# Performance work log

Hardware: AMD Instinct MI355X
Metric: run time of the kernel (lower is better)

## Reference

```python
import jax, jax.numpy as jnp
import numpy as np

SPLINE_ORDER = 3


def _bspline_basis(x, knots, k, order):
    """Cox-de Boor recursion with static (python float) knots, matching the torch code exactly."""
    if order == 0:
        if k + 1 >= len(knots):
            return jnp.zeros_like(x)
        return ((knots[k] <= x) & (x < knots[k + 1])).astype(x.dtype)
    left = 0.0
    right = 0.0
    if k + order < len(knots) and knots[k + order] != knots[k]:
        left = (x - knots[k]) / (knots[k + order] - knots[k]) * _bspline_basis(x, knots, k, order - 1)
    if k + order + 1 < len(knots) and knots[k + order + 1] != knots[k + 1]:
        right = (knots[k + order + 1] - x) / (knots[k + order + 1] - knots[k + 1]) * _bspline_basis(x, knots, k + 1, order - 1)
    return left + right


def setup_inputs() -> dict:
    key = jax.random.key(0)
    k1, k2, k3 = jax.random.split(key, 3)
    B, S, IN, OUT, NUM_KNOTS = 16, 4096, 256, 256, 5
    x = jax.random.normal(k1, (B, S, IN), dtype=jnp.float32)
    inner_coeffs = jax.random.normal(k2, (IN, NUM_KNOTS), dtype=jnp.float32) * 0.1
    outer_coeffs = jax.random.normal(k3, (OUT, IN), dtype=jnp.float32) * 0.1
    return {"x": x, "inner_coeffs": inner_coeffs, "outer_coeffs": outer_coeffs}


def reference(x, inner_coeffs, outer_coeffs):
    in_dim, num_knots = inner_coeffs.shape
    # knots = linspace(-1, 1, num_knots + spline_order), static python floats
    knots = np.linspace(-1.0, 1.0, num_knots + SPLINE_ORDER).tolist()
    xt = jnp.tanh(x)  # [B, S, I]
    # Original loops k in range(num_knots - spline_order); remaining basis columns stay zero,
    # so only the first n_active inner coefficients contribute.
    n_active = num_knots - SPLINE_ORDER
    basis = jnp.stack(
        [_bspline_basis(xt, knots, k, SPLINE_ORDER) for k in range(n_active)], axis=-1
    )  # [B, S, I, n_active]
    inner = jnp.einsum('bsik,ik->bsi', basis, inner_coeffs[:, :n_active])  # [B, S, I]
    return jnp.einsum('bsi,oi->bso', inner, outer_coeffs)  # [B, S, O]
```

## Files before the change

kernel.cpp:

```cpp
#include <hip/hip_runtime.h>
#include <hip/hip_bf16.h>
#include <stdint.h>


typedef __attribute__((ext_vector_type(8))) short short8;
typedef __attribute__((ext_vector_type(4))) float f32x4;

__device__ __forceinline__ uint16_t f2bf(float f) {
    union { float f; uint32_t u; } v; v.f = f;
    uint32_t r = v.u + 0x7FFFu + ((v.u >> 16) & 1u);
    return (uint16_t)(r >> 16);
}

__device__ __forceinline__ float cube_relu(float v) {
    float m = fmaxf(v, 0.0f);
    return m * m * m;
}

__device__ __forceinline__ float inner_eval(float xx, float c0, float c1) {
    float e  = __expf(2.0f * xx);
    float t  = 1.0f - 2.0f * __builtin_amdgcn_rcpf(e + 1.0f);
    float u  = (t + 1.0f) * 3.5f;
    float w0 = cube_relu(u);
    float w1 = cube_relu(u - 1.0f);
    float w2 = cube_relu(u - 2.0f);
    float w3 = cube_relu(u - 3.0f);
    float w4 = cube_relu(u - 4.0f);
    float w5 = cube_relu(u - 5.0f);
    float B0 = w0 - 4.0f*w1 + 6.0f*w2 - 4.0f*w3 + w4;
    float B1 = w1 - 4.0f*w2 + 6.0f*w3 - 4.0f*w4 + w5;
    return (c0 * B0 + c1 * B1) * (1.0f / 6.0f);
}

__device__ __forceinline__ void load_lds16(const void* g, void* l) {
    __builtin_amdgcn_global_load_lds(
        (const __attribute__((address_space(1))) uint32_t*)g,
        (__attribute__((address_space(3))) uint32_t*)l, 16, 0, 0);
}

__global__ void conv_w(const float4* __restrict__ wf, uint2* __restrict__ o) {
    const int i = blockIdx.x * blockDim.x + threadIdx.x;
    const float4 v = wf[i];
    uint2 r;
    r.x = (uint32_t)f2bf(v.x) | ((uint32_t)f2bf(v.y) << 16);
    r.y = (uint32_t)f2bf(v.z) | ((uint32_t)f2bf(v.w) << 16);
    o[i] = r;
}

#define SMEM_BYTES 22528

__global__ void kan_fused(const float* __restrict__ x,
                          const float* __restrict__ ic,
                          const uint16_t* __restrict__ wb,
                          float* __restrict__ out)
{
    __shared__ __align__(16) char smem[SMEM_BYTES];
    uint16_t* A_lds  = (uint16_t*)smem;
    char*     B_base = smem + 4096;
    float2*   C2     = (float2*)(smem + 20480);

    const int t    = threadIdx.x;
    const int lane = t & 63;
    const int w    = t >> 6;
    const int m0   = blockIdx.x * 64;

    C2[t] = make_float2(ic[t * 5 + 0], ic[t * 5 + 1]);

    f32x4 acc[4][4];
    #pragma unroll
    for (int i = 0; i < 4; ++i)
        #pragma unroll
        for (int j = 0; j < 4; ++j)
            acc[i][j] = (f32x4){0.f, 0.f, 0.f, 0.f};

    const int rowA = t >> 3;
    const int colA = (t & 7) << 2;
    const int mrow = lane & 15;
    const int quad = lane >> 4;

    #pragma unroll 1
    for (int kk = 0; kk < 8; ++kk) {
        __syncthreads();

        #pragma unroll
        for (int j = 0; j < 4; ++j) {
            const int f = ((w * 4 + j) << 10) + lane * 16;
            const int r = f >> 6;
            const int q = (f >> 4) & 3;
            load_lds16(wb + r * 256 + kk * 32 + q * 8, B_base + f);
        }

        #pragma unroll
        for (int j = 0; j < 2; ++j) {
            const int r  = rowA + j * 32;
            const int gk = kk * 32 + colA;
            const float4 xv = *(const float4*)(x + (size_t)(m0 + r) * 256 + gk);
            const float4 cA = *(const float4*)(&C2[gk]);
            const float4 cB = *(const float4*)(&C2[gk + 2]);
            float v0 = inner_eval(xv.x, cA.x, cA.y);
            float v1 = inner_eval(xv.y, cA.z, cA.w);
            float v2 = inner_eval(xv.z, cB.x, cB.y);
            float v3 = inner_eval(xv.w, cB.z, cB.w);
            uint32_t p0 = (uint32_t)f2bf(v0) | ((uint32_t)f2bf(v1) << 16);
            uint32_t p1 = (uint32_t)f2bf(v2) | ((uint32_t)f2bf(v3) << 16);
            *(uint2*)((char*)A_lds + (r * 32 + colA) * 2) = make_uint2(p0, p1);
        }

        __syncthreads();

        short8 a[4], b[4];
        #pragma unroll
        for (int i = 0; i < 4; ++i) {
            a[i] = *(const short8*)((const char*)A_lds + ((i * 16 + mrow) * 32 + quad * 8) * 2);
            b[i] = *(const short8*)(B_base + ((w * 64 + i * 16 + mrow) * 32 + quad * 8) * 2);
        }
        #pragma unroll
        for (int i = 0; i < 4; ++i)
            #pragma unroll
            for (int j = 0; j < 4; ++j)
                acc[i][j] = __builtin_amdgcn_mfma_f32_16x16x32_bf16(a[i], b[j], acc[i][j], 0, 0, 0);
    }

    #pragma unroll
    for (int i = 0; i < 4; ++i) {
        #pragma unroll
        for (int r = 0; r < 4; ++r) {
            const size_t row = (size_t)(m0 + i * 16 + quad * 4 + r);
            float* orow = out + row * 256 + w * 64 + mrow;
            #pragma unroll
            for (int j = 0; j < 4; ++j)
                orow[j * 16] = acc[i][j][r];
        }
    }
}

extern "C" void kernel_launch(void* const* d_in, const int* in_sizes, int n_in,
                              void* d_out, int out_size, void* d_ws, size_t ws_size,
                              hipStream_t stream) {
    const float* x  = (const float*)d_in[0];
    const float* ic = (const float*)d_in[1];
    const float* oc = (const float*)d_in[2];
    uint16_t* wb = (uint16_t*)d_ws;

    conv_w<<<64, 256, 0, stream>>>((const float4*)oc, (uint2*)wb);
    kan_fused<<<1024, 256, 0, stream>>>(x, ic, wb, (float*)d_out);
}
```

Measured before the change: 141.9 us.

## Drop LDS staging; each wave computes 16 rows by 256 outputs from registers

Reorganizes the fused kernel so each wave owns 16 rows and all 256 output columns. A-fragments come from the spline evaluation directly in registers, and B-fragments are loaded straight from global/L2 into registers. This removes the LDS A/B tiles and the per-iteration __syncthreads. The x loads are software-prefetched one k-step ahead, and packing uses the hardware bf16x2 conversion. In exchange each wave re-reads the entire weight matrix from L2, and the spline work is no longer shared across waves, which raises register pressure and cache traffic.

```diff
diff --git a/kernel.cpp b/kernel.cpp
--- a/kernel.cpp
+++ b/kernel.cpp
@@ -10,6 +10,12 @@
     union { float f; uint32_t u; } v; v.f = f;
     uint32_t r = v.u + 0x7FFFu + ((v.u >> 16) & 1u);
     return (uint16_t)(r >> 16);
+}
+
+__device__ __forceinline__ uint32_t pack_bf2(float lo, float hi) {
+    __hip_bfloat162 h = __float22bfloat162_rn(make_float2(lo, hi));
+    union { __hip_bfloat162 h; uint32_t u; } v; v.h = h;
+    return v.u;
 }
 
 __device__ __forceinline__ float cube_relu(float v) {
@@ -32,12 +38,6 @@
     return (c0 * B0 + c1 * B1) * (1.0f / 6.0f);
 }
 
-__device__ __forceinline__ void load_lds16(const void* g, void* l) {
-    __builtin_amdgcn_global_load_lds(
-        (const __attribute__((address_space(1))) uint32_t*)g,
-        (__attribute__((address_space(3))) uint32_t*)l, 16, 0, 0);
-}
-
 __global__ void conv_w(const float4* __restrict__ wf, uint2* __restrict__ o) {
     const int i = blockIdx.x * blockDim.x + threadIdx.x;
     const float4 v = wf[i];
@@ -47,90 +47,80 @@
     o[i] = r;
 }
 
-#define SMEM_BYTES 22528
-
-__global__ void kan_fused(const float* __restrict__ x,
-                          const float* __restrict__ ic,
-                          const uint16_t* __restrict__ wb,
-                          float* __restrict__ out)
+__global__ void __launch_bounds__(256) kan_fused(const float* __restrict__ x,
+                                                 const float* __restrict__ ic,
+                                                 const uint16_t* __restrict__ wb,
+                                                 float* __restrict__ out)
 {
-    __shared__ __align__(16) char smem[SMEM_BYTES];
-    uint16_t* A_lds  = (uint16_t*)smem;
-    char*     B_base = smem + 4096;
-    float2*   C2     = (float2*)(smem + 20480);
+    __shared__ __align__(16) float2 C2[256];
 
     const int t    = threadIdx.x;
     const int lane = t & 63;
     const int w    = t >> 6;
-    const int m0   = blockIdx.x * 64;
+    const int mrow = lane & 15;
+    const int quad = lane >> 4;
+    const int m    = blockIdx.x * 64 + w * 16 + mrow;
 
     C2[t] = make_float2(ic[t * 5 + 0], ic[t * 5 + 1]);
+    __syncthreads();
 
-    f32x4 acc[4][4];
+    f32x4 acc[16];
     #pragma unroll
-    for (int i = 0; i < 4; ++i)
-        #pragma unroll
-        for (int j = 0; j < 4; ++j)
-            acc[i][j] = (f32x4){0.f, 0.f, 0.f, 0.f};
+    for (int j = 0; j < 16; ++j) acc[j] = (f32x4){0.f, 0.f, 0.f, 0.f};
 
-    const int rowA = t >> 3;
-    const int colA = (t & 7) << 2;
-    const int mrow = lane & 15;
-    const int quad = lane >> 4;
+    const float*    xp = x  + (size_t)m * 256 + quad * 8;
+    const uint16_t* wp = wb + mrow * 256 + quad * 8;
+
+    float4 xa = *(const float4*)(xp + 0);
+    float4 xb = *(const float4*)(xp + 4);
 
     #pragma unroll 1
     for (int kk = 0; kk < 8; ++kk) {
-        __syncthreads();
+        short8 b[16];
+        #pragma unroll
+        for (int j = 0; j < 16; ++j)
+            b[j] = *(const short8*)(wp + j * 4096 + kk * 32);
+
+        float4 xa_n = xa, xb_n = xb;
+        if (kk < 7) {
+            xa_n = *(const float4*)(xp + kk * 32 + 32);
+            xb_n = *(const float4*)(xp + kk * 32 + 36);
+        }
+
+        const int gk = kk * 32 + quad * 8;
+        const float4 cA = *(const float4*)(&C2[gk + 0]);
+        const float4 cB = *(const float4*)(&C2[gk + 2]);
+        const float4 cC = *(const float4*)(&C2[gk + 4]);
+        const float4 cD = *(const float4*)(&C2[gk + 6]);
+
+        float v0 = inner_eval(xa.x, cA.x, cA.y);
+        float v1 = inner_eval(xa.y, cA.z, cA.w);
+        float v2 = inner_eval(xa.z, cB.x, cB.y);
+        float v3 = inner_eval(xa.w, cB.z, cB.w);
+        float v4 = inner_eval(xb.x, cC.x, cC.y);
+        float v5 = inner_eval(xb.y, cC.z, cC.w);
+        float v6 = inner_eval(xb.z, cD.x, cD.y);
+        float v7 = inner_eval(xb.w, cD.z, cD.w);
+
+        union { short8 v; uint32_t u[4]; } af;
+        af.u[0] = pack_bf2(v0, v1);
+        af.u[1] = pack_bf2(v2, v3);
+        af.u[2] = pack_bf2(v4, v5);
+        af.u[3] = pack_bf2(v6, v7);
 
         #pragma unroll
-        for (int j = 0; j < 4; ++j) {
-            const int f = ((w * 4 + j) << 10) + lane * 16;
-            const int r = f >> 6;
-            const int q = (f >> 4) & 3;
-            load_lds16(wb + r * 256 + kk * 32 + q * 8, B_base + f);
-        }
+        for (int j = 0; j < 16; ++j)
+            acc[j] = __builtin_amdgcn_mfma_f32_16x16x32_bf16(af.v, b[j], acc[j], 0, 0, 0);
 
-        #pragma unroll
-        for (int j = 0; j < 2; ++j) {
-            const int r  = rowA + j * 32;
-            const int gk = kk * 32 + colA;
-            const float4 xv = *(const float4*)(x + (size_t)(m0 + r) * 256 + gk);
-            const float4 cA = *(const float4*)(&C2[gk]);
-            const float4 cB = *(const float4*)(&C2[gk + 2]);
-            float v0 = inner_eval(xv.x, cA.x, cA.y);
-            float v1 = inner_eval(xv.y, cA.z, cA.w);
-            float v2 = inner_eval(xv.z, cB.x, cB.y);
-            float v3 = inner_eval(xv.w, cB.z, cB.w);
-            uint32_t p0 = (uint32_t)f2bf(v0) | ((uint32_t)f2bf(v1) << 16);
-            uint32_t p1 = (uint32_t)f2bf(v2) | ((uint32_t)f2bf(v3) << 16);
-            *(uint2*)((char*)A_lds + (r * 32 + colA) * 2) = make_uint2(p0, p1);
-        }
-
-        __syncthreads();
-
-        short8 a[4], b[4];
-        #pragma unroll
-        for (int i = 0; i < 4; ++i) {
-            a[i] = *(const short8*)((const char*)A_lds + ((i * 16 + mrow) * 32 + quad * 8) * 2);
-            b[i] = *(const short8*)(B_base + ((w * 64 + i * 16 + mrow) * 32 + quad * 8) * 2);
-        }
-        #pragma unroll
-        for (int i = 0; i < 4; ++i)
-            #pragma unroll
-            for (int j = 0; j < 4; ++j)
-                acc[i][j] = __builtin_amdgcn_mfma_f32_16x16x32_bf16(a[i], b[j], acc[i][j], 0, 0, 0);
+        xa = xa_n; xb = xb_n;
     }
 
+    float* op = out + (size_t)(blockIdx.x * 64 + w * 16 + quad * 4) * 256 + mrow;
     #pragma unroll
-    for (int i = 0; i < 4; ++i) {
+    for (int j = 0; j < 16; ++j) {
         #pragma unroll
-        for (int r = 0; r < 4; ++r) {
-            const size_t row = (size_t)(m0 + i * 16 + quad * 4 + r);
-            float* orow = out + row * 256 + w * 64 + mrow;
-            #pragma unroll
-            for (int j = 0; j < 4; ++j)
-                orow[j * 16] = acc[i][j][r];
-        }
+        for (int r = 0; r < 4; ++r)
+            op[(size_t)r * 256 + j * 16] = acc[j][r];
     }
 }
 
```

Measured after the change: 172.6 us. 1.22x slower.
